# Kernel optimization log

Hardware: AMD Instinct MI355X
Metric: run time of the kernel (lower is better)

The kernel has to match this reference:

```python
import jax, jax.numpy as jnp
import numpy as np

B = 8192
MAX_ATOMS = 768
EPS = 1e-7


def setup_inputs() -> dict:
    key = jax.random.key(0)
    k1, k2, k3 = jax.random.split(key, 3)
    inp = jax.random.normal(k1, (B, 3 * MAX_ATOMS), dtype=jnp.float32)
    tgt = jax.random.normal(k2, (B, 3 * MAX_ATOMS), dtype=jnp.float32)
    # variable atom counts; keep >= MAX_ATOMS//2 so centering/division is well-posed
    num_atoms = jax.random.randint(k3, (B,), MAX_ATOMS // 2, MAX_ATOMS + 1, dtype=jnp.int64)
    return {"input": inp, "target": tgt, "num_atoms": num_atoms}


def _kabsch_rmsd(inp, tgt, num_atoms):
    b = inp.shape[0]
    m = inp.shape[1] // 3
    X = inp.reshape(b, m, 3)
    Y = tgt.reshape(b, m, 3)
    mask = (jnp.arange(m)[None, :] < num_atoms[:, None])[..., None]  # [B, M, 1]
    n = num_atoms.astype(inp.dtype)[:, None]  # [B, 1]
    # center over the valid atoms of each sample
    Xc = (X - (jnp.where(mask, X, 0).sum(axis=1) / n)[:, None, :])
    Yc = (Y - (jnp.where(mask, Y, 0).sum(axis=1) / n)[:, None, :])
    Xc = jnp.where(mask, Xc, 0)
    Yc = jnp.where(mask, Yc, 0)
    # 3x3 correlation matrix per sample (Kabsch)
    R = jnp.einsum('bai,baj->bij', Xc, Yc)  # [B, 3, 3]
    s = jnp.linalg.svd(R, compute_uv=False)  # [B, 3], descending
    d = jnp.sign(jnp.linalg.det(R))  # proper-rotation correction
    trace = s[:, 0] + s[:, 1] + d * s[:, 2]
    e = jnp.sum(Xc * Xc, axis=(1, 2)) + jnp.sum(Yc * Yc, axis=(1, 2)) - 2.0 * trace
    n1 = num_atoms.astype(inp.dtype)
    return jnp.sqrt(jnp.maximum(e, 0.0) / n1 + EPS)


def reference(input, target, num_atoms):
    return _kabsch_rmsd(input, target, num_atoms)
```

## Files before the change

### kernel.cpp

```cpp
#include <hip/hip_runtime.h>
#include <math.h>

#ifndef M_PI
#define M_PI 3.14159265358979323846
#endif

#define MA 768
#define NB 8192

__device__ __forceinline__ float dpp_red_add(float v) {
    v += __int_as_float(__builtin_amdgcn_update_dpp(0, __float_as_int(v), 0x111, 0xf, 0xf, true));
    v += __int_as_float(__builtin_amdgcn_update_dpp(0, __float_as_int(v), 0x112, 0xf, 0xf, true));
    v += __int_as_float(__builtin_amdgcn_update_dpp(0, __float_as_int(v), 0x114, 0xf, 0xe, true));
    v += __int_as_float(__builtin_amdgcn_update_dpp(0, __float_as_int(v), 0x118, 0xf, 0xc, true));
    v += __int_as_float(__builtin_amdgcn_update_dpp(0, __float_as_int(v), 0x142, 0xa, 0xf, true));
    v += __int_as_float(__builtin_amdgcn_update_dpp(0, __float_as_int(v), 0x143, 0xc, 0xf, true));
    return v;
}

__global__ __launch_bounds__(256) void kabsch_reduce_kernel(
    const float* __restrict__ inp, const float* __restrict__ tgt,
    const int* __restrict__ natoms, float* __restrict__ ws)
{
    const int wave = threadIdx.x >> 6;
    const int lane = threadIdx.x & 63;
    const int b = blockIdx.x * 4 + wave;
    const int n = natoms[b];
    const float* __restrict__ X = inp + (size_t)b * (3 * MA);
    const float* __restrict__ Y = tgt + (size_t)b * (3 * MA);

    float sx0 = 0.f, sx1 = 0.f, sx2 = 0.f;
    float sy0 = 0.f, sy1 = 0.f, sy2 = 0.f;
    float c00 = 0.f, c01 = 0.f, c02 = 0.f;
    float c10 = 0.f, c11 = 0.f, c12 = 0.f;
    float c20 = 0.f, c21 = 0.f, c22 = 0.f;
    float nx2 = 0.f, ny2 = 0.f;

    auto acc = [&](float x0, float x1, float x2, float y0, float y1, float y2) {
        sx0 += x0; sx1 += x1; sx2 += x2;
        sy0 += y0; sy1 += y1; sy2 += y2;
        c00 = fmaf(x0, y0, c00); c01 = fmaf(x0, y1, c01); c02 = fmaf(x0, y2, c02);
        c10 = fmaf(x1, y0, c10); c11 = fmaf(x1, y1, c11); c12 = fmaf(x1, y2, c12);
        c20 = fmaf(x2, y0, c20); c21 = fmaf(x2, y1, c21); c22 = fmaf(x2, y2, c22);
        nx2 = fmaf(x0, x0, nx2); nx2 = fmaf(x1, x1, nx2); nx2 = fmaf(x2, x2, nx2);
        ny2 = fmaf(y0, y0, ny2); ny2 = fmaf(y1, y1, ny2); ny2 = fmaf(y2, y2, ny2);
    };

#pragma unroll
    for (int it = 0; it < 3; ++it) {
        const int base = it * 256 + lane * 4;
        if (base < n) {
            const float4* px = (const float4*)(X + 3 * base);
            const float4* py = (const float4*)(Y + 3 * base);
            float4 fx0 = px[0], fx1 = px[1], fx2 = px[2];
            float4 fy0 = py[0], fy1 = py[1], fy2 = py[2];

            acc(fx0.x, fx0.y, fx0.z, fy0.x, fy0.y, fy0.z);
            {
                bool v = (base + 1) < n;
                acc(v ? fx0.w : 0.f, v ? fx1.x : 0.f, v ? fx1.y : 0.f,
                    v ? fy0.w : 0.f, v ? fy1.x : 0.f, v ? fy1.y : 0.f);
            }
            {
                bool v = (base + 2) < n;
                acc(v ? fx1.z : 0.f, v ? fx1.w : 0.f, v ? fx2.x : 0.f,
                    v ? fy1.z : 0.f, v ? fy1.w : 0.f, v ? fy2.x : 0.f);
            }
            {
                bool v = (base + 3) < n;
                acc(v ? fx2.y : 0.f, v ? fx2.z : 0.f, v ? fx2.w : 0.f,
                    v ? fy2.y : 0.f, v ? fy2.z : 0.f, v ? fy2.w : 0.f);
            }
        }
    }

    sx0 = dpp_red_add(sx0); sx1 = dpp_red_add(sx1); sx2 = dpp_red_add(sx2);
    sy0 = dpp_red_add(sy0); sy1 = dpp_red_add(sy1); sy2 = dpp_red_add(sy2);
    c00 = dpp_red_add(c00); c01 = dpp_red_add(c01); c02 = dpp_red_add(c02);
    c10 = dpp_red_add(c10); c11 = dpp_red_add(c11); c12 = dpp_red_add(c12);
    c20 = dpp_red_add(c20); c21 = dpp_red_add(c21); c22 = dpp_red_add(c22);
    nx2 = dpp_red_add(nx2); ny2 = dpp_red_add(ny2);

    if (lane == 63) {
        ws[ 0 * NB + b] = sx0; ws[ 1 * NB + b] = sx1; ws[ 2 * NB + b] = sx2;
        ws[ 3 * NB + b] = sy0; ws[ 4 * NB + b] = sy1; ws[ 5 * NB + b] = sy2;
        ws[ 6 * NB + b] = c00; ws[ 7 * NB + b] = c01; ws[ 8 * NB + b] = c02;
        ws[ 9 * NB + b] = c10; ws[10 * NB + b] = c11; ws[11 * NB + b] = c12;
        ws[12 * NB + b] = c20; ws[13 * NB + b] = c21; ws[14 * NB + b] = c22;
        ws[15 * NB + b] = nx2; ws[16 * NB + b] = ny2;
    }
}

__global__ __launch_bounds__(256) void kabsch_finish_kernel(
    const float* __restrict__ ws, const int* __restrict__ natoms,
    float* __restrict__ out)
{
    const int b = blockIdx.x * 256 + threadIdx.x;
    const int n = natoms[b];
    const double dn = (double)n;

    const float sx0 = ws[ 0 * NB + b], sx1 = ws[ 1 * NB + b], sx2 = ws[ 2 * NB + b];
    const float sy0 = ws[ 3 * NB + b], sy1 = ws[ 4 * NB + b], sy2 = ws[ 5 * NB + b];
    const float c00 = ws[ 6 * NB + b], c01 = ws[ 7 * NB + b], c02 = ws[ 8 * NB + b];
    const float c10 = ws[ 9 * NB + b], c11 = ws[10 * NB + b], c12 = ws[11 * NB + b];
    const float c20 = ws[12 * NB + b], c21 = ws[13 * NB + b], c22 = ws[14 * NB + b];
    const float nx2 = ws[15 * NB + b], ny2 = ws[16 * NB + b];

    double R00 = (double)c00 - (double)sx0 * (double)sy0 / dn;
    double R01 = (double)c01 - (double)sx0 * (double)sy1 / dn;
    double R02 = (double)c02 - (double)sx0 * (double)sy2 / dn;
    double R10 = (double)c10 - (double)sx1 * (double)sy0 / dn;
    double R11 = (double)c11 - (double)sx1 * (double)sy1 / dn;
    double R12 = (double)c12 - (double)sx1 * (double)sy2 / dn;
    double R20 = (double)c20 - (double)sx2 * (double)sy0 / dn;
    double R21 = (double)c21 - (double)sx2 * (double)sy1 / dn;
    double R22 = (double)c22 - (double)sx2 * (double)sy2 / dn;
    double ex = (double)nx2 -
        ((double)sx0 * sx0 + (double)sx1 * sx1 + (double)sx2 * sx2) / dn;
    double ey = (double)ny2 -
        ((double)sy0 * sy0 + (double)sy1 * sy1 + (double)sy2 * sy2) / dn;

    double A00 = R00 * R00 + R10 * R10 + R20 * R20;
    double A11 = R01 * R01 + R11 * R11 + R21 * R21;
    double A22 = R02 * R02 + R12 * R12 + R22 * R22;
    double A01 = R00 * R01 + R10 * R11 + R20 * R21;
    double A02 = R00 * R02 + R10 * R12 + R20 * R22;
    double A12 = R01 * R02 + R11 * R12 + R21 * R22;

    double detR = R00 * (R11 * R22 - R12 * R21)
                - R01 * (R10 * R22 - R12 * R20)
                + R02 * (R10 * R21 - R11 * R20);

    double q = (A00 + A11 + A22) / 3.0;
    double p1 = A01 * A01 + A02 * A02 + A12 * A12;
    double b00 = A00 - q, b11 = A11 - q, b22 = A22 - q;
    double p2 = b00 * b00 + b11 * b11 + b22 * b22 + 2.0 * p1;
    double e0, e1, e2;
    if (p2 <= 0.0) {
        e0 = e1 = e2 = q;
    } else {
        double p = sqrt(p2 / 6.0);
        double ip = 1.0 / p;
        double B00 = b00 * ip, B11 = b11 * ip, B22 = b22 * ip;
        double B01 = A01 * ip, B02 = A02 * ip, B12 = A12 * ip;
        double detB = B00 * (B11 * B22 - B12 * B12)
                    - B01 * (B01 * B22 - B12 * B02)
                    + B02 * (B01 * B12 - B11 * B02);
        double r = 0.5 * detB;
        r = fmin(1.0, fmax(-1.0, r));
        double phi = acos(r) / 3.0;
        e0 = q + 2.0 * p * cos(phi);
        e2 = q + 2.0 * p * cos(phi + 2.0 * M_PI / 3.0);
        e1 = 3.0 * q - e0 - e2;
    }
    double s0 = sqrt(fmax(e0, 0.0));
    double s1 = sqrt(fmax(e1, 0.0));
    double s2 = sqrt(fmax(e2, 0.0));
    double d = (detR > 0.0) ? 1.0 : ((detR < 0.0) ? -1.0 : 0.0);
    double tr = s0 + s1 + d * s2;
    double e = ex + ey - 2.0 * tr;
    out[b] = (float)sqrt(fmax(e, 0.0) / dn + 1e-7);
}

extern "C" void kernel_launch(void* const* d_in, const int* in_sizes, int n_in,
                              void* d_out, int out_size, void* d_ws, size_t ws_size,
                              hipStream_t stream) {
    const float* inp = (const float*)d_in[0];
    const float* tgt = (const float*)d_in[1];
    const int* natoms = (const int*)d_in[2];
    float* out = (float*)d_out;
    float* ws = (float*)d_ws;
    (void)ws_size; (void)n_in; (void)in_sizes;
    kabsch_reduce_kernel<<<dim3(out_size / 4), dim3(256), 0, stream>>>(inp, tgt, natoms, ws);
    kabsch_finish_kernel<<<dim3(out_size / 256), dim3(256), 0, stream>>>(ws, natoms, out);
}
```

Measured before the change: 28.09 us.

## Load contiguous per-lane chunks, pack workspace per sample, cheapen finish math

The reduce kernel now has each lane load a contiguous 36-float chunk (12 atoms) of X and Y unconditionally into registers, then masks per atom. This replaces the strided three-iteration loop that skipped loads past n. The workspace becomes an array-of-structs with a stride of 20 floats, so it is written and read with float4 stores and loads. The finish kernel replaces the double divisions with a reciprocal multiply and uses float acosf/__cosf instead of double trig. Padded atoms are now always loaded, which adds memory traffic, and the float trig lowers eigenvalue precision.

```diff
diff --git a/kernel.cpp b/kernel.cpp
--- a/kernel.cpp
+++ b/kernel.cpp
@@ -7,6 +7,7 @@
 
 #define MA 768
 #define NB 8192
+#define WS_STRIDE 20
 
 __device__ __forceinline__ float dpp_red_add(float v) {
     v += __int_as_float(__builtin_amdgcn_update_dpp(0, __float_as_int(v), 0x111, 0xf, 0xf, true));
@@ -29,6 +30,17 @@
     const float* __restrict__ X = inp + (size_t)b * (3 * MA);
     const float* __restrict__ Y = tgt + (size_t)b * (3 * MA);
 
+    float ax[36], ay[36];
+    {
+        const float4* px = (const float4*)(X + 36 * lane);
+        const float4* py = (const float4*)(Y + 36 * lane);
+#pragma unroll
+        for (int k = 0; k < 9; ++k) {
+            *(float4*)&ax[4 * k] = px[k];
+            *(float4*)&ay[4 * k] = py[k];
+        }
+    }
+
     float sx0 = 0.f, sx1 = 0.f, sx2 = 0.f;
     float sy0 = 0.f, sy1 = 0.f, sy2 = 0.f;
     float c00 = 0.f, c01 = 0.f, c02 = 0.f;
@@ -36,7 +48,16 @@
     float c20 = 0.f, c21 = 0.f, c22 = 0.f;
     float nx2 = 0.f, ny2 = 0.f;
 
-    auto acc = [&](float x0, float x1, float x2, float y0, float y1, float y2) {
+    const int a0 = 12 * lane;
+#pragma unroll
+    for (int j = 0; j < 12; ++j) {
+        const bool v = (a0 + j) < n;
+        const float x0 = v ? ax[3 * j + 0] : 0.f;
+        const float x1 = v ? ax[3 * j + 1] : 0.f;
+        const float x2 = v ? ax[3 * j + 2] : 0.f;
+        const float y0 = v ? ay[3 * j + 0] : 0.f;
+        const float y1 = v ? ay[3 * j + 1] : 0.f;
+        const float y2 = v ? ay[3 * j + 2] : 0.f;
         sx0 += x0; sx1 += x1; sx2 += x2;
         sy0 += y0; sy1 += y1; sy2 += y2;
         c00 = fmaf(x0, y0, c00); c01 = fmaf(x0, y1, c01); c02 = fmaf(x0, y2, c02);
@@ -44,34 +65,6 @@
         c20 = fmaf(x2, y0, c20); c21 = fmaf(x2, y1, c21); c22 = fmaf(x2, y2, c22);
         nx2 = fmaf(x0, x0, nx2); nx2 = fmaf(x1, x1, nx2); nx2 = fmaf(x2, x2, nx2);
         ny2 = fmaf(y0, y0, ny2); ny2 = fmaf(y1, y1, ny2); ny2 = fmaf(y2, y2, ny2);
-    };
-
-#pragma unroll
-    for (int it = 0; it < 3; ++it) {
-        const int base = it * 256 + lane * 4;
-        if (base < n) {
-            const float4* px = (const float4*)(X + 3 * base);
-            const float4* py = (const float4*)(Y + 3 * base);
-            float4 fx0 = px[0], fx1 = px[1], fx2 = px[2];
-            float4 fy0 = py[0], fy1 = py[1], fy2 = py[2];
-
-            acc(fx0.x, fx0.y, fx0.z, fy0.x, fy0.y, fy0.z);
-            {
-                bool v = (base + 1) < n;
-                acc(v ? fx0.w : 0.f, v ? fx1.x : 0.f, v ? fx1.y : 0.f,
-                    v ? fy0.w : 0.f, v ? fy1.x : 0.f, v ? fy1.y : 0.f);
-            }
-            {
-                bool v = (base + 2) < n;
-                acc(v ? fx1.z : 0.f, v ? fx1.w : 0.f, v ? fx2.x : 0.f,
-                    v ? fy1.z : 0.f, v ? fy1.w : 0.f, v ? fy2.x : 0.f);
-            }
-            {
-                bool v = (base + 3) < n;
-                acc(v ? fx2.y : 0.f, v ? fx2.z : 0.f, v ? fx2.w : 0.f,
-                    v ? fy2.y : 0.f, v ? fy2.z : 0.f, v ? fy2.w : 0.f);
-            }
-        }
     }
 
     sx0 = dpp_red_add(sx0); sx1 = dpp_red_add(sx1); sx2 = dpp_red_add(sx2);
@@ -82,12 +75,12 @@
     nx2 = dpp_red_add(nx2); ny2 = dpp_red_add(ny2);
 
     if (lane == 63) {
-        ws[ 0 * NB + b] = sx0; ws[ 1 * NB + b] = sx1; ws[ 2 * NB + b] = sx2;
-        ws[ 3 * NB + b] = sy0; ws[ 4 * NB + b] = sy1; ws[ 5 * NB + b] = sy2;
-        ws[ 6 * NB + b] = c00; ws[ 7 * NB + b] = c01; ws[ 8 * NB + b] = c02;
-        ws[ 9 * NB + b] = c10; ws[10 * NB + b] = c11; ws[11 * NB + b] = c12;
-        ws[12 * NB + b] = c20; ws[13 * NB + b] = c21; ws[14 * NB + b] = c22;
-        ws[15 * NB + b] = nx2; ws[16 * NB + b] = ny2;
+        float4* pw = (float4*)(ws + (size_t)b * WS_STRIDE);
+        pw[0] = make_float4(sx0, sx1, sx2, sy0);
+        pw[1] = make_float4(sy1, sy2, c00, c01);
+        pw[2] = make_float4(c02, c10, c11, c12);
+        pw[3] = make_float4(c20, c21, c22, nx2);
+        pw[4] = make_float4(ny2, 0.f, 0.f, 0.f);
     }
 }
 
@@ -97,28 +90,29 @@
 {
     const int b = blockIdx.x * 256 + threadIdx.x;
     const int n = natoms[b];
-    const double dn = (double)n;
+    const double inv_n = 1.0 / (double)n;
 
-    const float sx0 = ws[ 0 * NB + b], sx1 = ws[ 1 * NB + b], sx2 = ws[ 2 * NB + b];
-    const float sy0 = ws[ 3 * NB + b], sy1 = ws[ 4 * NB + b], sy2 = ws[ 5 * NB + b];
-    const float c00 = ws[ 6 * NB + b], c01 = ws[ 7 * NB + b], c02 = ws[ 8 * NB + b];
-    const float c10 = ws[ 9 * NB + b], c11 = ws[10 * NB + b], c12 = ws[11 * NB + b];
-    const float c20 = ws[12 * NB + b], c21 = ws[13 * NB + b], c22 = ws[14 * NB + b];
-    const float nx2 = ws[15 * NB + b], ny2 = ws[16 * NB + b];
+    const float4* pw = (const float4*)(ws + (size_t)b * WS_STRIDE);
+    float4 w0 = pw[0], w1 = pw[1], w2 = pw[2], w3 = pw[3], w4 = pw[4];
+    const float sx0 = w0.x, sx1 = w0.y, sx2 = w0.z, sy0 = w0.w;
+    const float sy1 = w1.x, sy2 = w1.y, c00 = w1.z, c01 = w1.w;
+    const float c02 = w2.x, c10 = w2.y, c11 = w2.z, c12 = w2.w;
+    const float c20 = w3.x, c21 = w3.y, c22 = w3.z, nx2 = w3.w;
+    const float ny2 = w4.x;
 
-    double R00 = (double)c00 - (double)sx0 * (double)sy0 / dn;
-    double R01 = (double)c01 - (double)sx0 * (double)sy1 / dn;
-    double R02 = (double)c02 - (double)sx0 * (double)sy2 / dn;
-    double R10 = (double)c10 - (double)sx1 * (double)sy0 / dn;
-    double R11 = (double)c11 - (double)sx1 * (double)sy1 / dn;
-    double R12 = (double)c12 - (double)sx1 * (double)sy2 / dn;
-    double R20 = (double)c20 - (double)sx2 * (double)sy0 / dn;
-    double R21 = (double)c21 - (double)sx2 * (double)sy1 / dn;
-    double R22 = (double)c22 - (double)sx2 * (double)sy2 / dn;
+    double R00 = (double)c00 - (double)sx0 * (double)sy0 * inv_n;
+    double R01 = (double)c01 - (double)sx0 * (double)sy1 * inv_n;
+    double R02 = (double)c02 - (double)sx0 * (double)sy2 * inv_n;
+    double R10 = (double)c10 - (double)sx1 * (double)sy0 * inv_n;
+    double R11 = (double)c11 - (double)sx1 * (double)sy1 * inv_n;
+    double R12 = (double)c12 - (double)sx1 * (double)sy2 * inv_n;
+    double R20 = (double)c20 - (double)sx2 * (double)sy0 * inv_n;
+    double R21 = (double)c21 - (double)sx2 * (double)sy1 * inv_n;
+    double R22 = (double)c22 - (double)sx2 * (double)sy2 * inv_n;
     double ex = (double)nx2 -
-        ((double)sx0 * sx0 + (double)sx1 * sx1 + (double)sx2 * sx2) / dn;
+        ((double)sx0 * sx0 + (double)sx1 * sx1 + (double)sx2 * sx2) * inv_n;
     double ey = (double)ny2 -
-        ((double)sy0 * sy0 + (double)sy1 * sy1 + (double)sy2 * sy2) / dn;
+        ((double)sy0 * sy0 + (double)sy1 * sy1 + (double)sy2 * sy2) * inv_n;
 
     double A00 = R00 * R00 + R10 * R10 + R20 * R20;
     double A11 = R01 * R01 + R11 * R11 + R21 * R21;
@@ -148,9 +142,11 @@
                     + B02 * (B01 * B12 - B11 * B02);
         double r = 0.5 * detB;
         r = fmin(1.0, fmax(-1.0, r));
-        double phi = acos(r) / 3.0;
-        e0 = q + 2.0 * p * cos(phi);
-        e2 = q + 2.0 * p * cos(phi + 2.0 * M_PI / 3.0);
+        float phi = acosf((float)r) * (1.0f / 3.0f);
+        float cA = __cosf(phi);
+        float cC = __cosf(phi + (float)(2.0 * M_PI / 3.0));
+        e0 = q + 2.0 * p * (double)cA;
+        e2 = q + 2.0 * p * (double)cC;
         e1 = 3.0 * q - e0 - e2;
     }
     double s0 = sqrt(fmax(e0, 0.0));
@@ -159,7 +155,7 @@
     double d = (detR > 0.0) ? 1.0 : ((detR < 0.0) ? -1.0 : 0.0);
     double tr = s0 + s1 + d * s2;
     double e = ex + ey - 2.0 * tr;
-    out[b] = (float)sqrt(fmax(e, 0.0) / dn + 1e-7);
+    out[b] = (float)sqrt(fmax(e, 0.0) * inv_n + 1e-7);
 }
 
 extern "C" void kernel_launch(void* const* d_in, const int* in_sizes, int n_in,
```

New measurement: 31.99 us. 1.14x slower.
